# Kernel tuning notes

Measured on AMD Instinct MI355X. Metric: run time of the kernel, lower is better.

## Reference

```python
import jax, jax.numpy as jnp
import numpy as np

REFN, RN, G = 4, 2, 1          # reference views, query-group repeat, n_groups
NH, DH = 4, 32                 # heads, head channels
C = NH * DH                    # 128
H = W = 64
STRIDE, KS = 2, 3
HK, WK = H // STRIDE, W // STRIDE
L = 2048                       # query tokens per batch element
OFR = 2.0                      # offset_range_factor
SCALE = DH ** -0.5


def _grid_sample(img, grid):
    # img: (N, Ch, H, W); grid: (N, Hg, Wg, 2) xy in [-1,1]
    # bilinear, align_corners=True, padding_mode='zeros' (matches F.grid_sample)
    N, Ch, Hh, Ww = img.shape
    gx = (grid[..., 0] + 1.0) * 0.5 * (Ww - 1)
    gy = (grid[..., 1] + 1.0) * 0.5 * (Hh - 1)
    x0 = jnp.floor(gx); y0 = jnp.floor(gy)
    x1, y1 = x0 + 1.0, y0 + 1.0

    def gather(xi, yi):
        valid = ((xi >= 0) & (xi <= Ww - 1) & (yi >= 0) & (yi <= Hh - 1))
        xc = jnp.clip(xi, 0, Ww - 1).astype(jnp.int32)
        yc = jnp.clip(yi, 0, Hh - 1).astype(jnp.int32)
        g = jax.vmap(lambda im, yy, xx: im[:, yy, xx])(img, yc, xc)  # (N,Ch,Hg,Wg)
        return g * valid[:, None].astype(img.dtype)

    wa = (x1 - gx) * (y1 - gy); wb = (gx - x0) * (y1 - gy)
    wc = (x1 - gx) * (gy - y0); wd = (gx - x0) * (gy - y0)
    return (gather(x0, y0) * wa[:, None] + gather(x1, y0) * wb[:, None]
            + gather(x0, y1) * wc[:, None] + gather(x1, y1) * wd[:, None])


def setup_inputs():
    key = jax.random.key(0)
    ks = jax.random.split(key, 10)
    s = 0.05  # keep logits in a sane range with random weights
    return {
        "x": jax.random.normal(ks[0], (REFN, C, H, W), jnp.float32),
        "y": jax.random.normal(ks[1], (REFN, C, H, W), jnp.float32),
        "q_": jax.random.normal(ks[2], (RN * REFN, L, C), jnp.float32),
        "mask_": jnp.ones((RN * REFN, L, 1), jnp.float32),
        "Wq": jax.random.normal(ks[3], (C, C), jnp.float32) * s,
        "bq": jnp.zeros((C,), jnp.float32),
        "Wmd": jax.random.normal(ks[4], (C, C), jnp.float32) * s,
        "dw_w": jax.random.normal(ks[5], (C, 1, KS, KS), jnp.float32) * s,
        "dw_b": jnp.zeros((C,), jnp.float32),
        "ln_g": jnp.ones((C,), jnp.float32),
        "ln_b": jnp.zeros((C,), jnp.float32),
        "off_w": jax.random.normal(ks[6], (2, C), jnp.float32) * s,
        "Wk": jax.random.normal(ks[7], (C, C), jnp.float32) * s,
        "bk": jnp.zeros((C,), jnp.float32),
        "Wv": jax.random.normal(ks[8], (C, C), jnp.float32) * s,
        "bv": jnp.zeros((C,), jnp.float32),
        "Wo": jax.random.normal(ks[9], (C, C), jnp.float32) * s,
        "bo": jnp.zeros((C,), jnp.float32),
    }


def _forward(x, y, q_, mask_, Wq, bq, Wmd, dw_w, dw_b, ln_g, ln_b, off_w,
             Wk, bk, Wv, bv, Wo, bo):
    B = q_.shape[0]
    # masked mean over tokens -> modulation vector, then proj_q (Linear)
    q_cond = jnp.sum(q_ * mask_, 1) / (jnp.sum(mask_, 1) + 1e-6)   # (B, C)
    q_cond = q_cond @ Wq.T + bq

    xb = jnp.tile(x, (RN, 1, 1, 1))                                 # (B, C, H, W)

    # Conv2DMod (StyleGAN2 modulated 1x1 conv, demod eps 1e-8)
    wmod = Wmd[None] * (q_cond[:, None, :] + 1.0)                   # (B, Cout, Cin)
    wmod = wmod * jax.lax.rsqrt(jnp.sum(wmod * wmod, -1, keepdims=True) + 1e-8)
    q_t = jnp.einsum('boi,bihw->bohw', wmod, xb)                    # (B, C, H, W)

    # conv_offset: depthwise 3x3 s2 -> LayerNorm(channel) -> GELU -> 1x1 (no bias)
    t = jax.lax.conv_general_dilated(
        q_t, dw_w, (STRIDE, STRIDE), ((1, 1), (1, 1)),
        feature_group_count=C, dimension_numbers=('NCHW', 'OIHW', 'NCHW'))
    t = t + dw_b[None, :, None, None]
    mu = jnp.mean(t, 1, keepdims=True)
    var = jnp.mean((t - mu) ** 2, 1, keepdims=True)
    t = (t - mu) * jax.lax.rsqrt(var + 1e-5)
    t = t * ln_g[None, :, None, None] + ln_b[None, :, None, None]
    t = jax.nn.gelu(t, approximate=False)
    offset = jnp.einsum('oc,bchw->bohw', off_w, t)                  # (B*G, 2, HK, WK)

    orange = jnp.array([1.0 / (HK - 1), 1.0 / (WK - 1)], jnp.float32).reshape(1, 2, 1, 1)
    offset = jnp.tanh(offset) * orange * OFR
    offset = jnp.transpose(offset, (0, 2, 3, 1))                    # (B*G, HK, WK, 2) yx

    ry = (jnp.linspace(0.5, HK - 0.5, HK) / (HK - 1.0)) * 2.0 - 1.0
    rx = (jnp.linspace(0.5, WK - 0.5, WK) / (WK - 1.0)) * 2.0 - 1.0
    ref = jnp.stack(jnp.meshgrid(ry, rx, indexing='ij'), -1)        # (HK, WK, 2) yx
    ref = jnp.broadcast_to(ref[None], (B * G, HK, WK, 2))

    pos = offset + ref            # offset_range_factor >= 0 -> no clamp
    pos = pos[..., ::-1]          # yx -> xy for grid_sample
    ns = HK * WK
    # '(rn refn gn) h w n -> (refn gn) rn (h w) n'  (G == 1)
    grid = pos.reshape(RN, REFN, ns, 2).transpose(1, 0, 2, 3)       # (REFN, RN, ns, 2)

    xs = _grid_sample(y, grid)                                      # (REFN, C, RN, ns)
    # 'refn c (rn gn) (h w) -> (rn refn gn) c h w'  (G == 1)
    xs = xs.transpose(2, 0, 1, 3).reshape(B, C, ns)                 # (B, C, ns)

    k = (jnp.einsum('oc,bcn->bon', Wk, xs) + bk[None, :, None]).reshape(B * NH, DH, ns)
    v = (jnp.einsum('oc,bcn->bon', Wv, xs) + bv[None, :, None]).reshape(B * NH, DH, ns)
    q = jnp.transpose(q_, (0, 2, 1)).reshape(B * NH, DH, -1)        # (B*NH, DH, L)

    attn = jnp.einsum('bcm,bcn->bmn', q, k) * SCALE                 # (B*NH, L, ns)
    # NOTE: original calls attn.masked_fill(...) WITHOUT assignment (non in-place)
    # so the mask has no effect on attention -- faithfully omitted.
    attn = jax.nn.softmax(attn, axis=-1)
    out = jnp.einsum('bmn,bcn->bcm', attn, v)                       # (B*NH, DH, L)
    out = out.reshape(B, C, -1).transpose(0, 2, 1)                  # (B, L, C), G == 1
    yo = out @ Wo.T + bo
    return yo, grid.reshape(B, G, HK, WK, 2), ref.reshape(B, G, HK, WK, 2)


def reference(x, y, q_, mask_, Wq, bq, Wmd, dw_w, dw_b, ln_g, ln_b, off_w,
              Wk, bk, Wv, bv, Wo, bo):
    return _forward(x, y, q_, mask_, Wq, bq, Wmd, dw_w, dw_b, ln_g, ln_b, off_w,
                    Wk, bk, Wv, bv, Wo, bo)
```

## Files before the change

### kernel.cpp

```cpp
#include <hip/hip_runtime.h>
#include <math.h>


#define SCALE_F 0.17677669529663687f

typedef __attribute__((ext_vector_type(8))) short short8v;
typedef __attribute__((ext_vector_type(8))) unsigned short u16x8;
typedef __attribute__((ext_vector_type(4))) unsigned short u16x4;
typedef __attribute__((ext_vector_type(4))) float f32x4;

static __device__ __forceinline__ unsigned short f2bf(float f) {
  unsigned int u = __builtin_bit_cast(unsigned int, f);
  u += 0x7fffu + ((u >> 16) & 1u);
  return (unsigned short)(u >> 16);
}
static __device__ __forceinline__ float bf2f(unsigned short s) {
  unsigned int u = ((unsigned int)s) << 16;
  return __builtin_bit_cast(float, u);
}

__global__ void kt_pack(const float* __restrict__ y, const float* __restrict__ x,
                        float* __restrict__ y_t, unsigned short* __restrict__ xTb) {
  __shared__ __align__(16) float tile[128][65];
  int bid = blockIdx.x;
  int t = threadIdx.x;
  if (bid < 256) {
    int n = bid >> 6, yy = bid & 63;
    for (int p = 0; p < 32; ++p) {
      int idx = p * 256 + t;
      int c = idx >> 6, xx = idx & 63;
      tile[c][xx] = y[((n * 128 + c) * 64 + yy) * 64 + xx];
    }
    __syncthreads();
    for (int p = 0; p < 32; ++p) {
      int idx = p * 256 + t;
      int xx = idx >> 7, c = idx & 127;
      y_t[((n * 64 + yy) * 64 + xx) * 128 + c] = tile[c][xx];
    }
  } else {
    int nb = bid - 256;
    int n = nb >> 6, yy = nb & 63;
    for (int p = 0; p < 32; ++p) {
      int idx = p * 256 + t;
      int c = idx >> 6, xx = idx & 63;
      tile[c][xx] = x[((n * 128 + c) * 64 + yy) * 64 + xx];
    }
    __syncthreads();
    for (int p = 0; p < 4; ++p) {
      int idx = p * 256 + t;
      int xx = idx >> 4, g = idx & 15;
      u16x8 v;
#pragma unroll
      for (int j = 0; j < 8; ++j) v[j] = f2bf(tile[g * 8 + j][xx]);
      *reinterpret_cast<u16x8*>(
          xTb + ((size_t)n * 4096 + yy * 64 + xx) * 128 + g * 8) = v;
    }
  }
}

__global__ void k_qsum(const float* __restrict__ q_, const float* __restrict__ mask_,
                       float* __restrict__ qpart, float* __restrict__ mpart) {
  int b = blockIdx.x, ch = blockIdx.y, c = threadIdx.x;
  float acc = 0.f, ma = 0.f;
  for (int mm = 0; mm < 64; ++mm) {
    int m = ch * 64 + mm;
    float mk = mask_[b * 2048 + m];
    acc += q_[(b * 2048 + m) * 128 + c] * mk;
    ma += mk;
  }
  qpart[(b * 32 + ch) * 128 + c] = acc;
  if (c == 0) mpart[b * 32 + ch] = ma;
}

__global__ void k_wmod(const float* __restrict__ qpart, const float* __restrict__ mpart,
                       const float* __restrict__ Wq, const float* __restrict__ bq,
                       const float* __restrict__ Wmd, unsigned short* __restrict__ wmodb) {
  int b = blockIdx.x, c = threadIdx.x;
  __shared__ float qc[128], q2[128];
  float s = 0.f, ms = 0.f;
  for (int ch = 0; ch < 32; ++ch) {
    s += qpart[(b * 32 + ch) * 128 + c];
    ms += mpart[b * 32 + ch];
  }
  qc[c] = s / (ms + 1e-6f);
  __syncthreads();
  float acc = bq[c];
  for (int i = 0; i < 128; ++i) acc += qc[i] * Wq[c * 128 + i];
  q2[c] = acc + 1.0f;
  __syncthreads();
  float nrm = 0.f;
  for (int i = 0; i < 128; ++i) {
    float wv = Wmd[c * 128 + i] * q2[i];
    nrm += wv * wv;
  }
  float rs = 1.0f / sqrtf(nrm + 1e-8f);
  for (int i = 0; i < 128; ++i)
    wmodb[(b * 128 + c) * 128 + i] = f2bf(Wmd[c * 128 + i] * q2[i] * rs);
}

__global__ __launch_bounds__(256) void k_qt_mfma(
    const unsigned short* __restrict__ wmodb,
    const unsigned short* __restrict__ xTb,
    unsigned short* __restrict__ q_tb) {
  int b = blockIdx.x;
  int n0 = blockIdx.y * 128;
  int t = threadIdx.x;
  int w = t >> 6, l = t & 63;
  int lr = l & 15, lg = l >> 4;

  __shared__ __align__(16) unsigned short Asw[128 * 128];
  __shared__ __align__(16) unsigned short Bsw[128 * 128];
  char* Ab = reinterpret_cast<char*>(Asw);
  char* Bb = reinterpret_cast<char*>(Bsw);

  const unsigned short* asrc = wmodb + (size_t)b * 128 * 128;
  const unsigned short* bsrc = xTb + ((size_t)(b & 3) * 4096 + n0) * 128;
#pragma unroll
  for (int it = 0; it < 8; ++it) {
    int idx = it * 256 + t;
    int row = idx >> 4, cb = (idx & 15) * 16;
    int dst = row * 256 + (cb ^ ((row & 7) << 4));
    *reinterpret_cast<u16x8*>(Ab + dst) = *reinterpret_cast<const u16x8*>(asrc + idx * 8);
    *reinterpret_cast<u16x8*>(Bb + dst) = *reinterpret_cast<const u16x8*>(bsrc + idx * 8);
  }
  __syncthreads();

  const f32x4 z4 = {0.f, 0.f, 0.f, 0.f};
  f32x4 acc[8][2];
#pragma unroll
  for (int mf = 0; mf < 8; ++mf) { acc[mf][0] = z4; acc[mf][1] = z4; }

#pragma unroll
  for (int ks = 0; ks < 4; ++ks) {
    int cb = ks * 64 + lg * 16;
    short8v bf[2];
#pragma unroll
    for (int nf = 0; nf < 2; ++nf) {
      int row = w * 32 + nf * 16 + lr;
      bf[nf] = *reinterpret_cast<const short8v*>(Bb + row * 256 + (cb ^ ((row & 7) << 4)));
    }
#pragma unroll
    for (int mf = 0; mf < 8; ++mf) {
      int row = mf * 16 + lr;
      short8v af = *reinterpret_cast<const short8v*>(Ab + row * 256 + (cb ^ ((row & 7) << 4)));
      acc[mf][0] = __builtin_amdgcn_mfma_f32_16x16x32_bf16(af, bf[0], acc[mf][0], 0, 0, 0);
      acc[mf][1] = __builtin_amdgcn_mfma_f32_16x16x32_bf16(af, bf[1], acc[mf][1], 0, 0, 0);
    }
  }

#pragma unroll
  for (int mf = 0; mf < 8; ++mf)
#pragma unroll
    for (int nf = 0; nf < 2; ++nf)
#pragma unroll
      for (int r = 0; r < 4; ++r) {
        int o = mf * 16 + lg * 4 + r;
        int px = n0 + w * 32 + nf * 16 + lr;
        q_tb[((size_t)(b * 128 + o)) * 4096 + px] = f2bf(acc[mf][nf][r]);
      }
}

__global__ void k_dwconv(const unsigned short* __restrict__ q_tb,
                         const float* __restrict__ dw_w,
                         const float* __restrict__ dw_b, float* __restrict__ t0) {
  int bid = blockIdx.x;
  int t = threadIdx.x;
  int b = bid >> 9;
  int c = (bid >> 2) & 127;
  int px = (bid & 3) * 256 + t;
  int i = px >> 5, j = px & 31;
  float w[9];
#pragma unroll
  for (int q = 0; q < 9; ++q) w[q] = dw_w[c * 9 + q];
  const unsigned short* src = q_tb + (size_t)(b * 128 + c) * 4096;
  float acc = dw_b[c];
#pragma unroll
  for (int dy = 0; dy < 3; ++dy) {
    int yy = 2 * i - 1 + dy;
    if (yy < 0 || yy > 63) continue;
#pragma unroll
    for (int dx = 0; dx < 3; ++dx) {
      int xx = 2 * j - 1 + dx;
      if (xx < 0 || xx > 63) continue;
      acc += w[dy * 3 + dx] * bf2f(src[yy * 64 + xx]);
    }
  }
  t0[(b * 128 + c) * 1024 + px] = acc;
}

__global__ __launch_bounds__(256) void k_ln_off(
    const float* __restrict__ t0, const float* __restrict__ ln_g,
    const float* __restrict__ ln_b, const float* __restrict__ off_w,
    float* __restrict__ posg, float* __restrict__ grid_out,
    float* __restrict__ ref_out) {
  int b = blockIdx.x;
  int s0 = blockIdx.y * 64;
  int t = threadIdx.x;
  __shared__ float tile[128][64];
  __shared__ float red0[4][64], red1[4][64];

  for (int p = 0; p < 32; ++p) {
    int idx = p * 256 + t;
    int c = idx >> 6, s = idx & 63;
    tile[c][s] = t0[(b * 128 + c) * 1024 + s0 + s];
  }
  __syncthreads();

  int s = t & 63, cg = t >> 6;
  float sum = 0.f, sq = 0.f;
  for (int cc = 0; cc < 32; ++cc) {
    float v = tile[cg * 32 + cc][s];
    sum += v; sq += v * v;
  }
  red0[cg][s] = sum; red1[cg][s] = sq;
  __syncthreads();
  float tsum = red0[0][s] + red0[1][s] + red0[2][s] + red0[3][s];
  float tsq  = red1[0][s] + red1[1][s] + red1[2][s] + red1[3][s];
  float mu = tsum * (1.0f / 128.0f);
  float var = tsq * (1.0f / 128.0f) - mu * mu;
  float rstd = 1.0f / sqrtf(var + 1e-5f);
  float o0 = 0.f, o1 = 0.f;
  for (int cc = 0; cc < 32; ++cc) {
    int c = cg * 32 + cc;
    float v = tile[c][s];
    float xn = (v - mu) * rstd * ln_g[c] + ln_b[c];
    float g = 0.5f * xn * (1.0f + erff(xn * 0.7071067811865476f));
    o0 += off_w[c] * g;
    o1 += off_w[128 + c] * g;
  }
  __syncthreads();
  red0[cg][s] = o0; red1[cg][s] = o1;
  __syncthreads();
  if (t < 64) {
    float off0 = red0[0][s] + red0[1][s] + red0[2][s] + red0[3][s];
    float off1 = red1[0][s] + red1[1][s] + red1[2][s] + red1[3][s];
    float offy = tanhf(off0) * (1.0f / 31.0f) * 2.0f;
    float offx = tanhf(off1) * (1.0f / 31.0f) * 2.0f;
    int sg = s0 + s;
    int i = sg >> 5, j = sg & 31;
    float ry = (0.5f + (float)i) / 31.0f * 2.0f - 1.0f;
    float rx = (0.5f + (float)j) / 31.0f * 2.0f - 1.0f;
    float posy = offy + ry;
    float posx = offx + rx;
    int bp = (b & 3) * 2 + (b >> 2);
    float2 g2; g2.x = posx; g2.y = posy;
    *reinterpret_cast<float2*>(&grid_out[(bp * 1024 + sg) * 2]) = g2;
    float2 r2; r2.x = ry; r2.y = rx;
    *reinterpret_cast<float2*>(&ref_out[(b * 1024 + sg) * 2]) = r2;
    float2 p2;
    p2.x = (posx + 1.0f) * 0.5f * 63.0f;
    p2.y = (posy + 1.0f) * 0.5f * 63.0f;
    *reinterpret_cast<float2*>(&posg[(b * 1024 + sg) * 2]) = p2;
  }
}

__global__ void k_gsample(const float* __restrict__ y_t, const float* __restrict__ posg,
                          unsigned short* __restrict__ xsb) {
  int b = blockIdx.x;
  int s = blockIdx.y * 2 + (threadIdx.x >> 7);
  int c = threadIdx.x & 127;
  float gx = posg[(b * 1024 + s) * 2 + 0];
  float gy = posg[(b * 1024 + s) * 2 + 1];
  float x0 = floorf(gx), y0 = floorf(gy);
  float x1 = x0 + 1.0f, y1 = y0 + 1.0f;
  float wa = (x1 - gx) * (y1 - gy);
  float wb = (gx - x0) * (y1 - gy);
  float wc = (x1 - gx) * (gy - y0);
  float wd = (gx - x0) * (gy - y0);
  int n = b & 3;
  const float* base = y_t + n * 64 * 64 * 128 + c;
  float acc = 0.f;
  if (x0 >= 0.f && x0 <= 63.f && y0 >= 0.f && y0 <= 63.f)
    acc += wa * base[((int)y0 * 64 + (int)x0) * 128];
  if (x1 >= 0.f && x1 <= 63.f && y0 >= 0.f && y0 <= 63.f)
    acc += wb * base[((int)y0 * 64 + (int)x1) * 128];
  if (x0 >= 0.f && x0 <= 63.f && y1 >= 0.f && y1 <= 63.f)
    acc += wc * base[((int)y1 * 64 + (int)x0) * 128];
  if (x1 >= 0.f && x1 <= 63.f && y1 >= 0.f && y1 <= 63.f)
    acc += wd * base[((int)y1 * 64 + (int)x1) * 128];
  xsb[(b * 1024 + s) * 128 + c] = f2bf(acc);
}

__global__ __launch_bounds__(256) void k_projkv_mfma(
    const unsigned short* __restrict__ xsb, const float* __restrict__ Wk,
    const float* __restrict__ Wv, const float* __restrict__ bk,
    const float* __restrict__ bv, unsigned short* __restrict__ kb,
    unsigned short* __restrict__ vb) {
  int b = blockIdx.x, nt = blockIdx.y, z = blockIdx.z;
  int t = threadIdx.x;
  int w = t >> 6, l = t & 63;
  int lr = l & 15, lg = l >> 4;

  __shared__ __align__(16) unsigned short Asw[128 * 128];
  __shared__ __align__(16) unsigned short Bsw[128 * 128];
  char* Ab = reinterpret_cast<char*>(Asw);
  char* Bb = reinterpret_cast<char*>(Bsw);

  const float* asrcf = (z == 0) ? Wk : Wv;
  const unsigned short* bsrc = xsb + ((size_t)b * 1024 + nt * 128) * 128;
  const float* bias = (z == 0) ? bk : bv;
#pragma unroll
  for (int it = 0; it < 8; ++it) {
    int idx = it * 256 + t;
    int row = idx >> 4, cb = (idx & 15) * 16;
    int dst = row * 256 + (cb ^ ((row & 7) << 4));
    float4 f0 = *reinterpret_cast<const float4*>(asrcf + idx * 8);
    float4 f1 = *reinterpret_cast<const float4*>(asrcf + idx * 8 + 4);
    u16x8 av;
    av[0] = f2bf(f0.x); av[1] = f2bf(f0.y); av[2] = f2bf(f0.z); av[3] = f2bf(f0.w);
    av[4] = f2bf(f1.x); av[5] = f2bf(f1.y); av[6] = f2bf(f1.z); av[7] = f2bf(f1.w);
    *reinterpret_cast<u16x8*>(Ab + dst) = av;
    *reinterpret_cast<u16x8*>(Bb + dst) = *reinterpret_cast<const u16x8*>(bsrc + idx * 8);
  }
  __syncthreads();

  const f32x4 z4 = {0.f, 0.f, 0.f, 0.f};
  f32x4 acc[8][2];
#pragma unroll
  for (int mf = 0; mf < 8; ++mf) { acc[mf][0] = z4; acc[mf][1] = z4; }

#pragma unroll
  for (int ks = 0; ks < 4; ++ks) {
    int cb = ks * 64 + lg * 16;
    short8v bf[2];
#pragma unroll
    for (int nf = 0; nf < 2; ++nf) {
      int row = w * 32 + nf * 16 + lr;
      bf[nf] = *reinterpret_cast<const short8v*>(Bb + row * 256 + (cb ^ ((row & 7) << 4)));
    }
#pragma unroll
    for (int mf = 0; mf < 8; ++mf) {
      int row = mf * 16 + lr;
      short8v af = *reinterpret_cast<const short8v*>(Ab + row * 256 + (cb ^ ((row & 7) << 4)));
      acc[mf][0] = __builtin_amdgcn_mfma_f32_16x16x32_bf16(af, bf[0], acc[mf][0], 0, 0, 0);
      acc[mf][1] = __builtin_amdgcn_mfma_f32_16x16x32_bf16(af, bf[1], acc[mf][1], 0, 0, 0);
    }
  }

  if (z == 0) {
#pragma unroll
    for (int mf = 0; mf < 8; ++mf) {
      int o0 = mf * 16 + lg * 4;
      int h = o0 >> 5, d0 = o0 & 31;
#pragma unroll
      for (int nf = 0; nf < 2; ++nf) {
        int n = nt * 128 + w * 32 + nf * 16 + lr;
        u16x4 pk;
#pragma unroll
        for (int r = 0; r < 4; ++r) pk[r] = f2bf(acc[mf][nf][r] + bias[o0 + r]);
        *reinterpret_cast<u16x4*>(kb + ((size_t)(b * 4 + h) * 1024 + n) * 32 + d0) = pk;
      }
    }
  } else {
#pragma unroll
    for (int mf = 0; mf < 8; ++mf)
#pragma unroll
      for (int nf = 0; nf < 2; ++nf)
#pragma unroll
        for (int r = 0; r < 4; ++r) {
          int o = mf * 16 + lg * 4 + r;
          int n = nt * 128 + w * 32 + nf * 16 + lr;
          vb[(size_t)(b * 128 + o) * 1024 + n] = f2bf(acc[mf][nf][r] + bias[o]);
        }
  }
}

__global__ __launch_bounds__(256) void k_attn_mfma(
    const float* __restrict__ q_, const unsigned short* __restrict__ kb,
    const unsigned short* __restrict__ vb, unsigned short* __restrict__ obmcb) {
  int bh = blockIdx.x;
  int b = bh >> 2, h = bh & 3;
  int m0 = blockIdx.y * 128;
  int t = threadIdx.x;
  int w = t >> 6, l = t & 63;
  int lr = l & 15, lg = l >> 4;

  __shared__ __align__(16) unsigned short K_lds[2][2048];
  __shared__ __align__(16) unsigned short V_lds[2][2048];
  __shared__ __align__(16) unsigned short P_lds[8192];

  short8v qa[2];
#pragma unroll
  for (int mf = 0; mf < 2; ++mf) {
    int m = m0 + w * 32 + mf * 16 + lr;
    const float* qp = q_ + ((size_t)(b * 2048 + m)) * 128 + h * 32 + lg * 8;
    float4 x0 = *reinterpret_cast<const float4*>(qp);
    float4 x1 = *reinterpret_cast<const float4*>(qp + 4);
    float vals[8] = {x0.x, x0.y, x0.z, x0.w, x1.x, x1.y, x1.z, x1.w};
    short8v q8;
#pragma unroll
    for (int j = 0; j < 8; ++j) q8[j] = (short)f2bf(vals[j] * SCALE_F);
    qa[mf] = q8;
  }

  const unsigned short* kbase = kb + (size_t)bh * 1024 * 32;
  const unsigned short* vbase = vb + (size_t)bh * 32 * 1024;
  int ksl_n = t & 63, ksl_d = t >> 6;
  int vsl_d = t & 31, vsl_nb = t >> 5;

  u16x8 kreg = *reinterpret_cast<const u16x8*>(kbase + ((size_t)ksl_n) * 32 + ksl_d * 8);
  u16x8 vreg = *reinterpret_cast<const u16x8*>(vbase + (size_t)vsl_d * 1024 + vsl_nb * 8);
  *reinterpret_cast<u16x8*>(&K_lds[0][t * 8]) = kreg;
  *reinterpret_cast<u16x8*>(&V_lds[0][t * 8]) = vreg;
  __syncthreads();

  const f32x4 z4 = {0.f, 0.f, 0.f, 0.f};
  f32x4 oacc[2][2];
  float lsum[2][4];
#pragma unroll
  for (int mf = 0; mf < 2; ++mf) {
#pragma unroll
    for (int df = 0; df < 2; ++df) oacc[mf][df] = z4;
#pragma unroll
    for (int r = 0; r < 4; ++r) lsum[mf][r] = 0.f;
  }

  int swzW = ((lr >> 3) & 1) << 3;
  int swzR = (lg & 1) << 3;
  int cur = 0;
  for (int nt = 0; nt < 16; ++nt) {
    if (nt < 15) {
      kreg = *reinterpret_cast<const u16x8*>(
          kbase + ((size_t)((nt + 1) * 64 + ksl_n)) * 32 + ksl_d * 8);
      vreg = *reinterpret_cast<const u16x8*>(
          vbase + (size_t)vsl_d * 1024 + (nt + 1) * 64 + vsl_nb * 8);
    }

    short8v kfr[4];
#pragma unroll
    for (int nf = 0; nf < 4; ++nf)
      kfr[nf] = *reinterpret_cast<const short8v*>(&K_lds[cur][(lg * 64 + nf * 16 + lr) * 8]);
    f32x4 s[2][4];
#pragma unroll
    for (int mf = 0; mf < 2; ++mf)
#pragma unroll
      for (int nf = 0; nf < 4; ++nf)
        s[mf][nf] = __builtin_amdgcn_mfma_f32_16x16x32_bf16(qa[mf], kfr[nf], z4, 0, 0, 0);

#pragma unroll
    for (int mf = 0; mf < 2; ++mf) {
#pragma unroll
      for (int nf = 0; nf < 4; ++nf) {
        int sbase = (w * 256 + (nf * 2 + (lr >> 3)) * 32 + mf * 16 + lg * 4) * 8 + (lr & 7);
#pragma unroll
        for (int r = 0; r < 4; ++r) {
          float pe = __expf(s[mf][nf][r]);
          lsum[mf][r] += pe;
          P_lds[(sbase + r * 8) ^ swzW] = f2bf(pe);
        }
      }
    }

#pragma unroll
    for (int ks = 0; ks < 2; ++ks) {
      short8v pa[2], vf[2];
#pragma unroll
      for (int mf = 0; mf < 2; ++mf)
        pa[mf] = *reinterpret_cast<const short8v*>(
            &P_lds[((w * 256 + (ks * 4 + lg) * 32 + mf * 16 + lr) * 8) ^ swzR]);
#pragma unroll
      for (int df = 0; df < 2; ++df)
        vf[df] = *reinterpret_cast<const short8v*>(
            &V_lds[cur][((ks * 4 + lg) * 32 + df * 16 + lr) * 8]);
#pragma unroll
      for (int mf = 0; mf < 2; ++mf)
#pragma unroll
        for (int df = 0; df < 2; ++df)
          oacc[mf][df] = __builtin_amdgcn_mfma_f32_16x16x32_bf16(pa[mf], vf[df], oacc[mf][df], 0, 0, 0);
    }

    if (nt < 15) {
      *reinterpret_cast<u16x8*>(&K_lds[cur ^ 1][t * 8]) = kreg;
      *reinterpret_cast<u16x8*>(&V_lds[cur ^ 1][t * 8]) = vreg;
      __syncthreads();
      cur ^= 1;
    }
  }

#pragma unroll
  for (int mf = 0; mf < 2; ++mf) {
#pragma unroll
    for (int r = 0; r < 4; ++r) {
      float v = lsum[mf][r];
      v += __shfl_xor(v, 1); v += __shfl_xor(v, 2);
      v += __shfl_xor(v, 4); v += __shfl_xor(v, 8);
      float inv = 1.0f / v;
      int m = m0 + w * 32 + mf * 16 + lg * 4 + r;
      unsigned short* op = obmcb + ((size_t)(b * 2048 + m)) * 128 + h * 32;
      op[lr] = f2bf(oacc[mf][0][r] * inv);
      op[16 + lr] = f2bf(oacc[mf][1][r] * inv);
    }
  }
}

__global__ __launch_bounds__(256) void k_out_mfma(
    const unsigned short* __restrict__ obmcb, const float* __restrict__ Wo,
    const float* __restrict__ bo, float* __restrict__ yo) {
  int b = blockIdx.x, mt = blockIdx.y;
  int t = threadIdx.x;
  int w = t >> 6, l = t & 63;
  int lr = l & 15, lg = l >> 4;

  __shared__ __align__(16) unsigned short Asw[128 * 128];
  __shared__ __align__(16) unsigned short Bsw[128 * 128];
  char* Ab = reinterpret_cast<char*>(Asw);
  char* Bb = reinterpret_cast<char*>(Bsw);

  const unsigned short* bsrc = obmcb + ((size_t)b * 2048 + mt * 128) * 128;
#pragma unroll
  for (int it = 0; it < 8; ++it) {
    int idx = it * 256 + t;
    int row = idx >> 4, cb = (idx & 15) * 16;
    int dst = row * 256 + (cb ^ ((row & 7) << 4));
    float4 f0 = *reinterpret_cast<const float4*>(Wo + idx * 8);
    float4 f1 = *reinterpret_cast<const float4*>(Wo + idx * 8 + 4);
    u16x8 av;
    av[0] = f2bf(f0.x); av[1] = f2bf(f0.y); av[2] = f2bf(f0.z); av[3] = f2bf(f0.w);
    av[4] = f2bf(f1.x); av[5] = f2bf(f1.y); av[6] = f2bf(f1.z); av[7] = f2bf(f1.w);
    *reinterpret_cast<u16x8*>(Ab + dst) = av;
    *reinterpret_cast<u16x8*>(Bb + dst) = *reinterpret_cast<const u16x8*>(bsrc + idx * 8);
  }
  __syncthreads();

  const f32x4 z4 = {0.f, 0.f, 0.f, 0.f};
  f32x4 acc[8][2];
#pragma unroll
  for (int mf = 0; mf < 8; ++mf) { acc[mf][0] = z4; acc[mf][1] = z4; }

#pragma unroll
  for (int ks = 0; ks < 4; ++ks) {
    int cb = ks * 64 + lg * 16;
    short8v bf[2];
#pragma unroll
    for (int nf = 0; nf < 2; ++nf) {
      int row = w * 32 + nf * 16 + lr;
      bf[nf] = *reinterpret_cast<const short8v*>(Bb + row * 256 + (cb ^ ((row & 7) << 4)));
    }
#pragma unroll
    for (int mf = 0; mf < 8; ++mf) {
      int row = mf * 16 + lr;
      short8v af = *reinterpret_cast<const short8v*>(Ab + row * 256 + (cb ^ ((row & 7) << 4)));
      acc[mf][0] = __builtin_amdgcn_mfma_f32_16x16x32_bf16(af, bf[0], acc[mf][0], 0, 0, 0);
      acc[mf][1] = __builtin_amdgcn_mfma_f32_16x16x32_bf16(af, bf[1], acc[mf][1], 0, 0, 0);
    }
  }

#pragma unroll
  for (int mf = 0; mf < 8; ++mf) {
    int o0 = mf * 16 + lg * 4;
#pragma unroll
    for (int nf = 0; nf < 2; ++nf) {
      int m = mt * 128 + w * 32 + nf * 16 + lr;
      float4 rv;
      rv.x = acc[mf][nf][0] + bo[o0 + 0];
      rv.y = acc[mf][nf][1] + bo[o0 + 1];
      rv.z = acc[mf][nf][2] + bo[o0 + 2];
      rv.w = acc[mf][nf][3] + bo[o0 + 3];
      *reinterpret_cast<float4*>(&yo[((size_t)(b * 2048 + m)) * 128 + o0]) = rv;
    }
  }
}

extern "C" void kernel_launch(void* const* d_in, const int* in_sizes, int n_in,
                              void* d_out, int out_size, void* d_ws, size_t ws_size,
                              hipStream_t stream) {
  const float* x     = (const float*)d_in[0];
  const float* y     = (const float*)d_in[1];
  const float* q_    = (const float*)d_in[2];
  const float* mask_ = (const float*)d_in[3];
  const float* Wq    = (const float*)d_in[4];
  const float* bq    = (const float*)d_in[5];
  const float* Wmd   = (const float*)d_in[6];
  const float* dw_w  = (const float*)d_in[7];
  const float* dw_b  = (const float*)d_in[8];
  const float* ln_g  = (const float*)d_in[9];
  const float* ln_b  = (const float*)d_in[10];
  const float* off_w = (const float*)d_in[11];
  const float* Wk    = (const float*)d_in[12];
  const float* bk    = (const float*)d_in[13];
  const float* Wv    = (const float*)d_in[14];
  const float* bv    = (const float*)d_in[15];
  const float* Wo    = (const float*)d_in[16];
  const float* bo    = (const float*)d_in[17];

  float* out = (float*)d_out;
  float* yo       = out;
  float* grid_out = out + 2097152;
  float* ref_out  = grid_out + 16384;

  float* ws    = (float*)d_ws;
  float* y_t   = ws;
  float* qpart = y_t + 2097152;
  float* mpart = qpart + 32768;
  float* t0    = mpart + 256;
  float* posg  = t0 + 1048576;
  unsigned short* kbb   = (unsigned short*)(posg + 16384);
  unsigned short* vbb   = kbb + 1048576;
  unsigned short* xTb   = vbb + 1048576;
  unsigned short* wmodb = xTb + 2097152;
  unsigned short* xsb   = wmodb + 131072;
  unsigned short* obmcb = xsb + 1048576;
  unsigned short* q_tb  = obmcb + 2097152;

  hipLaunchKernelGGL(kt_pack, dim3(512), dim3(256), 0, stream, y, x, y_t, xTb);
  hipLaunchKernelGGL(k_qsum, dim3(8, 32), dim3(128), 0, stream, q_, mask_, qpart, mpart);
  hipLaunchKernelGGL(k_wmod, dim3(8), dim3(128), 0, stream,
                     qpart, mpart, Wq, bq, Wmd, wmodb);
  hipLaunchKernelGGL(k_qt_mfma, dim3(8, 32), dim3(256), 0, stream, wmodb, xTb, q_tb);
  hipLaunchKernelGGL(k_dwconv, dim3(4096), dim3(256), 0, stream, q_tb, dw_w, dw_b, t0);
  hipLaunchKernelGGL(k_ln_off, dim3(8, 16), dim3(256), 0, stream,
                     t0, ln_g, ln_b, off_w, posg, grid_out, ref_out);
  hipLaunchKernelGGL(k_gsample, dim3(8, 512), dim3(256), 0, stream, y_t, posg, xsb);
  hipLaunchKernelGGL(k_projkv_mfma, dim3(8, 8, 2), dim3(256), 0, stream,
                     xsb, Wk, Wv, bk, bv, kbb, vbb);
  hipLaunchKernelGGL(k_attn_mfma, dim3(32, 16), dim3(256), 0, stream, q_, kbb, vbb, obmcb);
  hipLaunchKernelGGL(k_out_mfma, dim3(8, 16), dim3(256), 0, stream, obmcb, Wo, bo, yo);
}
```

Before: 183.5 us.

## Fuse pack/qsum and dwconv/layernorm/offset/gridsample kernels to cut launches

Folds the query-mean partial sums into the transpose/pack kernel, so k_stage1 has 768 blocks. It widens k_wmod to 512 threads with split reductions. It also merges depthwise conv, layernorm, offset prediction and grid sampling into one kernel per (batch, output row). This removes four launches and the t0/posg round trips through global memory. The cost is a small fused grid of 256 blocks with more serial work per block, which may lower occupancy and parallelism for the dwconv and grid-sample stages.

```diff
diff --git a/kernel.cpp b/kernel.cpp
--- a/kernel.cpp
+++ b/kernel.cpp
@@ -19,8 +19,11 @@
   return __builtin_bit_cast(float, u);
 }
 
-__global__ void kt_pack(const float* __restrict__ y, const float* __restrict__ x,
-                        float* __restrict__ y_t, unsigned short* __restrict__ xTb) {
+__global__ __launch_bounds__(256) void k_stage1(
+    const float* __restrict__ y, const float* __restrict__ x,
+    const float* __restrict__ q_, const float* __restrict__ mask_,
+    float* __restrict__ y_t, unsigned short* __restrict__ xTb,
+    float* __restrict__ qpart, float* __restrict__ mpart) {
   __shared__ __align__(16) float tile[128][65];
   int bid = blockIdx.x;
   int t = threadIdx.x;
@@ -37,7 +40,7 @@
       int xx = idx >> 7, c = idx & 127;
       y_t[((n * 64 + yy) * 64 + xx) * 128 + c] = tile[c][xx];
     }
-  } else {
+  } else if (bid < 512) {
     int nb = bid - 256;
     int n = nb >> 6, yy = nb & 63;
     for (int p = 0; p < 32; ++p) {
@@ -55,46 +58,57 @@
       *reinterpret_cast<u16x8*>(
           xTb + ((size_t)n * 4096 + yy * 64 + xx) * 128 + g * 8) = v;
     }
-  }
-}
-
-__global__ void k_qsum(const float* __restrict__ q_, const float* __restrict__ mask_,
-                       float* __restrict__ qpart, float* __restrict__ mpart) {
-  int b = blockIdx.x, ch = blockIdx.y, c = threadIdx.x;
-  float acc = 0.f, ma = 0.f;
-  for (int mm = 0; mm < 64; ++mm) {
-    int m = ch * 64 + mm;
-    float mk = mask_[b * 2048 + m];
-    acc += q_[(b * 2048 + m) * 128 + c] * mk;
-    ma += mk;
-  }
-  qpart[(b * 32 + ch) * 128 + c] = acc;
-  if (c == 0) mpart[b * 32 + ch] = ma;
-}
-
-__global__ void k_wmod(const float* __restrict__ qpart, const float* __restrict__ mpart,
-                       const float* __restrict__ Wq, const float* __restrict__ bq,
-                       const float* __restrict__ Wmd, unsigned short* __restrict__ wmodb) {
-  int b = blockIdx.x, c = threadIdx.x;
-  __shared__ float qc[128], q2[128];
-  float s = 0.f, ms = 0.f;
-  for (int ch = 0; ch < 32; ++ch) {
-    s += qpart[(b * 32 + ch) * 128 + c];
-    ms += mpart[b * 32 + ch];
-  }
-  qc[c] = s / (ms + 1e-6f);
-  __syncthreads();
-  float acc = bq[c];
-  for (int i = 0; i < 128; ++i) acc += qc[i] * Wq[c * 128 + i];
-  q2[c] = acc + 1.0f;
-  __syncthreads();
-  float nrm = 0.f;
-  for (int i = 0; i < 128; ++i) {
+  } else {
+    int idx = bid - 512;
+    int b = idx >> 5, ch = idx & 31;
+    int c = t & 127, hh = t >> 7;
+    float acc = 0.f, ma = 0.f;
+    for (int mm = 0; mm < 32; ++mm) {
+      int m = ch * 64 + hh * 32 + mm;
+      float mk = mask_[b * 2048 + m];
+      acc += q_[(b * 2048 + m) * 128 + c] * mk;
+      ma += mk;
+    }
+    qpart[(b * 64 + ch * 2 + hh) * 128 + c] = acc;
+    if (c == 0) mpart[b * 64 + ch * 2 + hh] = ma;
+  }
+}
+
+__global__ __launch_bounds__(512) void k_wmod(
+    const float* __restrict__ qpart, const float* __restrict__ mpart,
+    const float* __restrict__ Wq, const float* __restrict__ bq,
+    const float* __restrict__ Wmd, unsigned short* __restrict__ wmodb) {
+  int b = blockIdx.x;
+  int t = threadIdx.x;
+  int c = t & 127, qq = t >> 7;
+  __shared__ float qc[128], q2[128], red[4][128];
+
+  float s = 0.f;
+  for (int ch = qq; ch < 64; ch += 4) s += qpart[(b * 64 + ch) * 128 + c];
+  red[qq][c] = s;
+  __syncthreads();
+  if (t < 128) {
+    float ms = 0.f;
+    for (int ch = 0; ch < 64; ++ch) ms += mpart[b * 64 + ch];
+    qc[c] = (red[0][c] + red[1][c] + red[2][c] + red[3][c]) / (ms + 1e-6f);
+  }
+  __syncthreads();
+  float a = 0.f;
+  for (int i = qq * 32; i < qq * 32 + 32; ++i) a += qc[i] * Wq[c * 128 + i];
+  red[qq][c] = a;
+  __syncthreads();
+  if (t < 128)
+    q2[c] = red[0][c] + red[1][c] + red[2][c] + red[3][c] + bq[c] + 1.0f;
+  __syncthreads();
+  float nr = 0.f;
+  for (int i = qq * 32; i < qq * 32 + 32; ++i) {
     float wv = Wmd[c * 128 + i] * q2[i];
-    nrm += wv * wv;
-  }
-  float rs = 1.0f / sqrtf(nrm + 1e-8f);
-  for (int i = 0; i < 128; ++i)
+    nr += wv * wv;
+  }
+  red[qq][c] = nr;
+  __syncthreads();
+  float rs = rsqrtf(red[0][c] + red[1][c] + red[2][c] + red[3][c] + 1e-8f);
+  for (int i = qq * 32; i < qq * 32 + 32; ++i)
     wmodb[(b * 128 + c) * 128 + i] = f2bf(Wmd[c * 128 + i] * q2[i] * rs);
 }
 
@@ -160,125 +174,107 @@
       }
 }
 
-__global__ void k_dwconv(const unsigned short* __restrict__ q_tb,
-                         const float* __restrict__ dw_w,
-                         const float* __restrict__ dw_b, float* __restrict__ t0) {
-  int bid = blockIdx.x;
+__global__ __launch_bounds__(256) void k_dlg(
+    const unsigned short* __restrict__ q_tb, const float* __restrict__ dw_w,
+    const float* __restrict__ dw_b, const float* __restrict__ ln_g,
+    const float* __restrict__ ln_b, const float* __restrict__ off_w,
+    const float* __restrict__ y_t, unsigned short* __restrict__ xsb,
+    float* __restrict__ grid_out, float* __restrict__ ref_out) {
+  int b = blockIdx.x, i = blockIdx.y;
   int t = threadIdx.x;
-  int b = bid >> 9;
-  int c = (bid >> 2) & 127;
-  int px = (bid & 3) * 256 + t;
-  int i = px >> 5, j = px & 31;
-  float w[9];
-#pragma unroll
-  for (int q = 0; q < 9; ++q) w[q] = dw_w[c * 9 + q];
-  const unsigned short* src = q_tb + (size_t)(b * 128 + c) * 4096;
-  float acc = dw_b[c];
-#pragma unroll
-  for (int dy = 0; dy < 3; ++dy) {
-    int yy = 2 * i - 1 + dy;
-    if (yy < 0 || yy > 63) continue;
-#pragma unroll
-    for (int dx = 0; dx < 3; ++dx) {
-      int xx = 2 * j - 1 + dx;
-      if (xx < 0 || xx > 63) continue;
-      acc += w[dy * 3 + dx] * bf2f(src[yy * 64 + xx]);
-    }
-  }
-  t0[(b * 128 + c) * 1024 + px] = acc;
-}
-
-__global__ __launch_bounds__(256) void k_ln_off(
-    const float* __restrict__ t0, const float* __restrict__ ln_g,
-    const float* __restrict__ ln_b, const float* __restrict__ off_w,
-    float* __restrict__ posg, float* __restrict__ grid_out,
-    float* __restrict__ ref_out) {
-  int b = blockIdx.x;
-  int s0 = blockIdx.y * 64;
-  int t = threadIdx.x;
-  __shared__ float tile[128][64];
-  __shared__ float red0[4][64], red1[4][64];
-
-  for (int p = 0; p < 32; ++p) {
+  __shared__ float tile[128][33];
+  __shared__ float red0[8][32], red1[8][32];
+  __shared__ float psx[32], psy[32];
+
+  for (int p = 0; p < 16; ++p) {
     int idx = p * 256 + t;
-    int c = idx >> 6, s = idx & 63;
-    tile[c][s] = t0[(b * 128 + c) * 1024 + s0 + s];
-  }
-  __syncthreads();
-
-  int s = t & 63, cg = t >> 6;
+    int c = idx >> 5, j = idx & 31;
+    const unsigned short* src = q_tb + (size_t)(b * 128 + c) * 4096;
+    float acc = dw_b[c];
+#pragma unroll
+    for (int dy = 0; dy < 3; ++dy) {
+      int yy = 2 * i - 1 + dy;
+      if (yy < 0 || yy > 63) continue;
+#pragma unroll
+      for (int dx = 0; dx < 3; ++dx) {
+        int xx = 2 * j - 1 + dx;
+        if (xx < 0 || xx > 63) continue;
+        acc += dw_w[c * 9 + dy * 3 + dx] * bf2f(src[yy * 64 + xx]);
+      }
+    }
+    tile[c][j] = acc;
+  }
+  __syncthreads();
+
+  int j = t & 31, cg = t >> 5;
   float sum = 0.f, sq = 0.f;
-  for (int cc = 0; cc < 32; ++cc) {
-    float v = tile[cg * 32 + cc][s];
+  for (int cc = 0; cc < 16; ++cc) {
+    float v = tile[cg * 16 + cc][j];
     sum += v; sq += v * v;
   }
-  red0[cg][s] = sum; red1[cg][s] = sq;
-  __syncthreads();
-  float tsum = red0[0][s] + red0[1][s] + red0[2][s] + red0[3][s];
-  float tsq  = red1[0][s] + red1[1][s] + red1[2][s] + red1[3][s];
+  red0[cg][j] = sum; red1[cg][j] = sq;
+  __syncthreads();
+  float tsum = 0.f, tsq = 0.f;
+#pragma unroll
+  for (int g = 0; g < 8; ++g) { tsum += red0[g][j]; tsq += red1[g][j]; }
   float mu = tsum * (1.0f / 128.0f);
   float var = tsq * (1.0f / 128.0f) - mu * mu;
   float rstd = 1.0f / sqrtf(var + 1e-5f);
   float o0 = 0.f, o1 = 0.f;
-  for (int cc = 0; cc < 32; ++cc) {
-    int c = cg * 32 + cc;
-    float v = tile[c][s];
-    float xn = (v - mu) * rstd * ln_g[c] + ln_b[c];
+  for (int cc = 0; cc < 16; ++cc) {
+    int c = cg * 16 + cc;
+    float xn = (tile[c][j] - mu) * rstd * ln_g[c] + ln_b[c];
     float g = 0.5f * xn * (1.0f + erff(xn * 0.7071067811865476f));
     o0 += off_w[c] * g;
     o1 += off_w[128 + c] * g;
   }
   __syncthreads();
-  red0[cg][s] = o0; red1[cg][s] = o1;
-  __syncthreads();
-  if (t < 64) {
-    float off0 = red0[0][s] + red0[1][s] + red0[2][s] + red0[3][s];
-    float off1 = red1[0][s] + red1[1][s] + red1[2][s] + red1[3][s];
+  red0[cg][j] = o0; red1[cg][j] = o1;
+  __syncthreads();
+  if (t < 32) {
+    float off0 = 0.f, off1 = 0.f;
+#pragma unroll
+    for (int g = 0; g < 8; ++g) { off0 += red0[g][t]; off1 += red1[g][t]; }
     float offy = tanhf(off0) * (1.0f / 31.0f) * 2.0f;
     float offx = tanhf(off1) * (1.0f / 31.0f) * 2.0f;
-    int sg = s0 + s;
-    int i = sg >> 5, j = sg & 31;
     float ry = (0.5f + (float)i) / 31.0f * 2.0f - 1.0f;
-    float rx = (0.5f + (float)j) / 31.0f * 2.0f - 1.0f;
+    float rx = (0.5f + (float)t) / 31.0f * 2.0f - 1.0f;
     float posy = offy + ry;
     float posx = offx + rx;
+    int sg = i * 32 + t;
     int bp = (b & 3) * 2 + (b >> 2);
     float2 g2; g2.x = posx; g2.y = posy;
     *reinterpret_cast<float2*>(&grid_out[(bp * 1024 + sg) * 2]) = g2;
     float2 r2; r2.x = ry; r2.y = rx;
     *reinterpret_cast<float2*>(&ref_out[(b * 1024 + sg) * 2]) = r2;
-    float2 p2;
-    p2.x = (posx + 1.0f) * 0.5f * 63.0f;
-    p2.y = (posy + 1.0f) * 0.5f * 63.0f;
-    *reinterpret_cast<float2*>(&posg[(b * 1024 + sg) * 2]) = p2;
-  }
-}
-
-__global__ void k_gsample(const float* __restrict__ y_t, const float* __restrict__ posg,
-                          unsigned short* __restrict__ xsb) {
-  int b = blockIdx.x;
-  int s = blockIdx.y * 2 + (threadIdx.x >> 7);
-  int c = threadIdx.x & 127;
-  float gx = posg[(b * 1024 + s) * 2 + 0];
-  float gy = posg[(b * 1024 + s) * 2 + 1];
-  float x0 = floorf(gx), y0 = floorf(gy);
-  float x1 = x0 + 1.0f, y1 = y0 + 1.0f;
-  float wa = (x1 - gx) * (y1 - gy);
-  float wb = (gx - x0) * (y1 - gy);
-  float wc = (x1 - gx) * (gy - y0);
-  float wd = (gx - x0) * (gy - y0);
+    psx[t] = (posx + 1.0f) * 0.5f * 63.0f;
+    psy[t] = (posy + 1.0f) * 0.5f * 63.0f;
+  }
+  __syncthreads();
+
   int n = b & 3;
-  const float* base = y_t + n * 64 * 64 * 128 + c;
-  float acc = 0.f;
-  if (x0 >= 0.f && x0 <= 63.f && y0 >= 0.f && y0 <= 63.f)
-    acc += wa * base[((int)y0 * 64 + (int)x0) * 128];
-  if (x1 >= 0.f && x1 <= 63.f && y0 >= 0.f && y0 <= 63.f)
-    acc += wb * base[((int)y0 * 64 + (int)x1) * 128];
-  if (x0 >= 0.f && x0 <= 63.f && y1 >= 0.f && y1 <= 63.f)
-    acc += wc * base[((int)y1 * 64 + (int)x0) * 128];
-  if (x1 >= 0.f && x1 <= 63.f && y1 >= 0.f && y1 <= 63.f)
-    acc += wd * base[((int)y1 * 64 + (int)x1) * 128];
-  xsb[(b * 1024 + s) * 128 + c] = f2bf(acc);
+  for (int p = 0; p < 16; ++p) {
+    int idx = p * 256 + t;
+    int c = idx & 127, px = idx >> 7;
+    float gx = psx[px], gy = psy[px];
+    float x0 = floorf(gx), y0 = floorf(gy);
+    float x1 = x0 + 1.0f, y1 = y0 + 1.0f;
+    float wa = (x1 - gx) * (y1 - gy);
+    float wb = (gx - x0) * (y1 - gy);
+    float wc = (x1 - gx) * (gy - y0);
+    float wd = (gx - x0) * (gy - y0);
+    const float* base = y_t + n * 64 * 64 * 128 + c;
+    float acc = 0.f;
+    if (x0 >= 0.f && x0 <= 63.f && y0 >= 0.f && y0 <= 63.f)
+      acc += wa * base[((int)y0 * 64 + (int)x0) * 128];
+    if (x1 >= 0.f && x1 <= 63.f && y0 >= 0.f && y0 <= 63.f)
+      acc += wb * base[((int)y0 * 64 + (int)x1) * 128];
+    if (x0 >= 0.f && x0 <= 63.f && y1 >= 0.f && y1 <= 63.f)
+      acc += wc * base[((int)y1 * 64 + (int)x0) * 128];
+    if (x1 >= 0.f && x1 <= 63.f && y1 >= 0.f && y1 <= 63.f)
+      acc += wd * base[((int)y1 * 64 + (int)x1) * 128];
+    xsb[((size_t)b * 1024 + i * 32 + px) * 128 + c] = f2bf(acc);
+  }
 }
 
 __global__ __launch_bounds__(256) void k_projkv_mfma(
@@ -591,10 +587,8 @@
   float* ws    = (float*)d_ws;
   float* y_t   = ws;
   float* qpart = y_t + 2097152;
-  float* mpart = qpart + 32768;
-  float* t0    = mpart + 256;
-  float* posg  = t0 + 1048576;
-  unsigned short* kbb   = (unsigned short*)(posg + 16384);
+  float* mpart = qpart + 65536;
+  unsigned short* kbb   = (unsigned short*)(mpart + 512);
   unsigned short* vbb   = kbb + 1048576;
   unsigned short* xTb   = vbb + 1048576;
   unsigned short* wmodb = xTb + 2097152;
@@ -602,15 +596,13 @@
   unsigned short* obmcb = xsb + 1048576;
   unsigned short* q_tb  = obmcb + 2097152;
 
-  hipLaunchKernelGGL(kt_pack, dim3(512), dim3(256), 0, stream, y, x, y_t, xTb);
-  hipLaunchKernelGGL(k_qsum, dim3(8, 32), dim3(128), 0, stream, q_, mask_, qpart, mpart);
-  hipLaunchKernelGGL(k_wmod, dim3(8), dim3(128), 0, stream,
+  hipLaunchKernelGGL(k_stage1, dim3(768), dim3(256), 0, stream,
+                     y, x, q_, mask_, y_t, xTb, qpart, mpart);
+  hipLaunchKernelGGL(k_wmod, dim3(8), dim3(512), 0, stream,
                      qpart, mpart, Wq, bq, Wmd, wmodb);
   hipLaunchKernelGGL(k_qt_mfma, dim3(8, 32), dim3(256), 0, stream, wmodb, xTb, q_tb);
-  hipLaunchKernelGGL(k_dwconv, dim3(4096), dim3(256), 0, stream, q_tb, dw_w, dw_b, t0);
-  hipLaunchKernelGGL(k_ln_off, dim3(8, 16), dim3(256), 0, stream,
-                     t0, ln_g, ln_b, off_w, posg, grid_out, ref_out);
-  hipLaunchKernelGGL(k_gsample, dim3(8, 512), dim3(256), 0, stream, y_t, posg, xsb);
+  hipLaunchKernelGGL(k_dlg, dim3(8, 32), dim3(256), 0, stream,
+                     q_tb, dw_w, dw_b, ln_g, ln_b, off_w, y_t, xsb, grid_out, ref_out);
   hipLaunchKernelGGL(k_projkv_mfma, dim3(8, 8, 2), dim3(256), 0, stream,
                      xsb, Wk, Wv, bk, bv, kbb, vbb);
   hipLaunchKernelGGL(k_attn_mfma, dim3(32, 16), dim3(256), 0, stream, q_, kbb, vbb, obmcb);
```

Result: slower. 199.6 us (+8.7%).

## Fuse query-sum into pack kernel and widen weight-modulation kernel to 512 threads

Applied to the files above, without the earlier changes.

Merges the masked query reduction into the transpose/pack kernel as extra blocks, so one launch does both and the independent work runs concurrently. The query-sum blocks now use 256 threads, each half covering 32 rows, which doubles the partial buffers. The weight-modulation kernel moves from 128 to 512 threads with a shared-memory reduction over four partial sums, aiming to shorten its serial per-thread loops. It adds extra barriers and reduction steps, and the workspace offsets shift to fit the larger partial buffers.

```diff
diff --git a/kernel.cpp b/kernel.cpp
--- a/kernel.cpp
+++ b/kernel.cpp
@@ -19,8 +19,11 @@
   return __builtin_bit_cast(float, u);
 }
 
-__global__ void kt_pack(const float* __restrict__ y, const float* __restrict__ x,
-                        float* __restrict__ y_t, unsigned short* __restrict__ xTb) {
+__global__ __launch_bounds__(256) void k_stage1(
+    const float* __restrict__ y, const float* __restrict__ x,
+    const float* __restrict__ q_, const float* __restrict__ mask_,
+    float* __restrict__ y_t, unsigned short* __restrict__ xTb,
+    float* __restrict__ qpart, float* __restrict__ mpart) {
   __shared__ __align__(16) float tile[128][65];
   int bid = blockIdx.x;
   int t = threadIdx.x;
@@ -37,7 +40,7 @@
       int xx = idx >> 7, c = idx & 127;
       y_t[((n * 64 + yy) * 64 + xx) * 128 + c] = tile[c][xx];
     }
-  } else {
+  } else if (bid < 512) {
     int nb = bid - 256;
     int n = nb >> 6, yy = nb & 63;
     for (int p = 0; p < 32; ++p) {
@@ -55,46 +58,57 @@
       *reinterpret_cast<u16x8*>(
           xTb + ((size_t)n * 4096 + yy * 64 + xx) * 128 + g * 8) = v;
     }
-  }
-}
-
-__global__ void k_qsum(const float* __restrict__ q_, const float* __restrict__ mask_,
-                       float* __restrict__ qpart, float* __restrict__ mpart) {
-  int b = blockIdx.x, ch = blockIdx.y, c = threadIdx.x;
-  float acc = 0.f, ma = 0.f;
-  for (int mm = 0; mm < 64; ++mm) {
-    int m = ch * 64 + mm;
-    float mk = mask_[b * 2048 + m];
-    acc += q_[(b * 2048 + m) * 128 + c] * mk;
-    ma += mk;
-  }
-  qpart[(b * 32 + ch) * 128 + c] = acc;
-  if (c == 0) mpart[b * 32 + ch] = ma;
-}
-
-__global__ void k_wmod(const float* __restrict__ qpart, const float* __restrict__ mpart,
-                       const float* __restrict__ Wq, const float* __restrict__ bq,
-                       const float* __restrict__ Wmd, unsigned short* __restrict__ wmodb) {
-  int b = blockIdx.x, c = threadIdx.x;
-  __shared__ float qc[128], q2[128];
-  float s = 0.f, ms = 0.f;
-  for (int ch = 0; ch < 32; ++ch) {
-    s += qpart[(b * 32 + ch) * 128 + c];
-    ms += mpart[b * 32 + ch];
-  }
-  qc[c] = s / (ms + 1e-6f);
-  __syncthreads();
-  float acc = bq[c];
-  for (int i = 0; i < 128; ++i) acc += qc[i] * Wq[c * 128 + i];
-  q2[c] = acc + 1.0f;
-  __syncthreads();
-  float nrm = 0.f;
-  for (int i = 0; i < 128; ++i) {
+  } else {
+    int idx = bid - 512;
+    int b = idx >> 5, ch = idx & 31;
+    int c = t & 127, hh = t >> 7;
+    float acc = 0.f, ma = 0.f;
+    for (int mm = 0; mm < 32; ++mm) {
+      int m = ch * 64 + hh * 32 + mm;
+      float mk = mask_[b * 2048 + m];
+      acc += q_[(b * 2048 + m) * 128 + c] * mk;
+      ma += mk;
+    }
+    qpart[(b * 64 + ch * 2 + hh) * 128 + c] = acc;
+    if (c == 0) mpart[b * 64 + ch * 2 + hh] = ma;
+  }
+}
+
+__global__ __launch_bounds__(512) void k_wmod(
+    const float* __restrict__ qpart, const float* __restrict__ mpart,
+    const float* __restrict__ Wq, const float* __restrict__ bq,
+    const float* __restrict__ Wmd, unsigned short* __restrict__ wmodb) {
+  int b = blockIdx.x;
+  int t = threadIdx.x;
+  int c = t & 127, qq = t >> 7;
+  __shared__ float qc[128], q2[128], red[4][128];
+
+  float s = 0.f;
+  for (int ch = qq; ch < 64; ch += 4) s += qpart[(b * 64 + ch) * 128 + c];
+  red[qq][c] = s;
+  __syncthreads();
+  if (t < 128) {
+    float ms = 0.f;
+    for (int ch = 0; ch < 64; ++ch) ms += mpart[b * 64 + ch];
+    qc[c] = (red[0][c] + red[1][c] + red[2][c] + red[3][c]) / (ms + 1e-6f);
+  }
+  __syncthreads();
+  float a = 0.f;
+  for (int i = qq * 32; i < qq * 32 + 32; ++i) a += qc[i] * Wq[c * 128 + i];
+  red[qq][c] = a;
+  __syncthreads();
+  if (t < 128)
+    q2[c] = red[0][c] + red[1][c] + red[2][c] + red[3][c] + bq[c] + 1.0f;
+  __syncthreads();
+  float nr = 0.f;
+  for (int i = qq * 32; i < qq * 32 + 32; ++i) {
     float wv = Wmd[c * 128 + i] * q2[i];
-    nrm += wv * wv;
-  }
-  float rs = 1.0f / sqrtf(nrm + 1e-8f);
-  for (int i = 0; i < 128; ++i)
+    nr += wv * wv;
+  }
+  red[qq][c] = nr;
+  __syncthreads();
+  float rs = rsqrtf(red[0][c] + red[1][c] + red[2][c] + red[3][c] + 1e-8f);
+  for (int i = qq * 32; i < qq * 32 + 32; ++i)
     wmodb[(b * 128 + c) * 128 + i] = f2bf(Wmd[c * 128 + i] * q2[i] * rs);
 }
 
@@ -591,8 +605,8 @@
   float* ws    = (float*)d_ws;
   float* y_t   = ws;
   float* qpart = y_t + 2097152;
-  float* mpart = qpart + 32768;
-  float* t0    = mpart + 256;
+  float* mpart = qpart + 65536;
+  float* t0    = mpart + 512;
   float* posg  = t0 + 1048576;
   unsigned short* kbb   = (unsigned short*)(posg + 16384);
   unsigned short* vbb   = kbb + 1048576;
@@ -602,9 +616,9 @@
   unsigned short* obmcb = xsb + 1048576;
   unsigned short* q_tb  = obmcb + 2097152;
 
-  hipLaunchKernelGGL(kt_pack, dim3(512), dim3(256), 0, stream, y, x, y_t, xTb);
-  hipLaunchKernelGGL(k_qsum, dim3(8, 32), dim3(128), 0, stream, q_, mask_, qpart, mpart);
-  hipLaunchKernelGGL(k_wmod, dim3(8), dim3(128), 0, stream,
+  hipLaunchKernelGGL(k_stage1, dim3(768), dim3(256), 0, stream,
+                     y, x, q_, mask_, y_t, xTb, qpart, mpart);
+  hipLaunchKernelGGL(k_wmod, dim3(8), dim3(512), 0, stream,
                      qpart, mpart, Wq, bq, Wmd, wmodb);
   hipLaunchKernelGGL(k_qt_mfma, dim3(8, 32), dim3(256), 0, stream, wmodb, xTb, q_tb);
   hipLaunchKernelGGL(k_dwconv, dim3(4096), dim3(256), 0, stream, q_tb, dw_w, dw_b, t0);
```

New measurement: 180.1 us. No clear change (-1.8%).
